# Kernel optimization log

Hardware: AMD Instinct MI355X
Metric: run time of the kernel (lower is better)

## Reference

```python
import jax, jax.numpy as jnp
import numpy as np
import math

N_HEAD = 16  # from init_kwargs

def setup_inputs() -> dict:
    key = jax.random.key(0)
    ks = jax.random.split(key, 11)
    B, T, D = 2, 2048, 1024
    s = 0.02
    return {
        "q": jax.random.normal(ks[0], (B, T, D), jnp.float32),
        "k": jax.random.normal(ks[1], (B, T, D), jnp.float32),
        "v": jax.random.normal(ks[2], (B, T, D), jnp.float32),
        "Wq": jax.random.normal(ks[3], (D, D), jnp.float32) * s,
        "bq": jax.random.normal(ks[4], (D,), jnp.float32) * s,
        "Wk": jax.random.normal(ks[5], (D, D), jnp.float32) * s,
        "bk": jax.random.normal(ks[6], (D,), jnp.float32) * s,
        "Wv": jax.random.normal(ks[7], (D, D), jnp.float32) * s,
        "bv": jax.random.normal(ks[8], (D,), jnp.float32) * s,
        "Wc": jax.random.normal(ks[9], (D, D), jnp.float32) * s,
        "bc": jax.random.normal(ks[10], (D,), jnp.float32) * s,
    }

def reference(q, k, v, Wq, bq, Wk, bk, Wv, bv, Wc, bc):
    B, T, D = q.shape
    H = N_HEAD
    nd = D // H

    def proj(x, W, b):
        # torch Linear: x @ W.T + b; then split heads -> [b, h, t, nd]
        y = x @ W.T + b
        return y.reshape(B, T, H, nd).transpose(0, 2, 1, 3)

    qh = proj(q, Wq, bq)
    kh = proj(k, Wk, bk)
    vh = proj(v, Wv, bv)

    # scores: [b, h, t_q, t_k]
    z = jnp.einsum('bhqd,bhkd->bhqk', qh, kh) / math.sqrt(nd)
    mask = jnp.tril(jnp.ones((T, T), dtype=bool))  # causal
    z = jnp.where(mask, z, -jnp.inf)
    # NOTE: original uses nn.Softmax(dim=-2) -> softmax over the QUERY axis
    attn = jax.nn.softmax(z, axis=-2)
    out = jnp.einsum('bhqk,bhkd->bhqd', attn, vh)  # [b, h, t, nd]
    out = out.transpose(0, 2, 1, 3).reshape(B, T, D)
    return out @ Wc.T + bc
```

## Files before the change

kernel.cpp:

```cpp
#include <hip/hip_runtime.h>


#define Dd 1024
#define Tt 2048
#define Bb 2
#define Hh 16
#define NDh 64
#define Mm (Bb * Tt)

using u16 = unsigned short;
using u32 = unsigned int;
typedef __attribute__((ext_vector_type(8))) short bf16x8;
typedef __attribute__((ext_vector_type(4))) float f32x4;

__device__ __forceinline__ u16 f2bf(float f) {
  return (u16)((__float_as_uint(f) + 0x8000u) >> 16);
}
__device__ __forceinline__ float fexp2(float x) {
  return __builtin_amdgcn_exp2f(x);
}
__device__ __forceinline__ void ldsdma16(const u16* g, u16* l) {
  __builtin_amdgcn_global_load_lds(
      (const __attribute__((address_space(1))) u32*)g,
      (__attribute__((address_space(3))) u32*)l, 16, 0, 0);
}
#define MFMA(a, b, c) __builtin_amdgcn_mfma_f32_16x16x32_bf16((a), (b), (c), 0, 0, 0)
__device__ __forceinline__ bf16x8 ldfrag(const u16* lds, int row, int kgrp) {
  return *(const bf16x8*)(lds + row * 64 + (((kgrp) ^ (row & 7)) * 8));
}

__global__ __launch_bounds__(256) void cvt_all(
    const float* __restrict__ w0, const float* __restrict__ w1,
    const float* __restrict__ w2, const float* __restrict__ w3,
    const float* __restrict__ q, const float* __restrict__ k,
    const float* __restrict__ v,
    u16* __restrict__ Wb, u16* __restrict__ Xb,
    float* __restrict__ outz, float* __restrict__ lsumz)
{
  const int vid = blockIdx.x * 256 + threadIdx.x;
  const float* s;
  u16* d;
  if (vid < (1 << 20)) {
    const int seg = vid >> 18, off = (vid & 0x3FFFF) * 4;
    s = (seg == 0 ? w0 : seg == 1 ? w1 : seg == 2 ? w2 : w3) + off;
    d = Wb + (size_t)seg * Dd * Dd + off;
    *(float4*)(outz + (size_t)vid * 4) = make_float4(0.f, 0.f, 0.f, 0.f);
    if (vid < Bb * Hh * Tt / 4)
      *(float4*)(lsumz + (size_t)vid * 4) = make_float4(0.f, 0.f, 0.f, 0.f);
  } else {
    const int iv = vid - (1 << 20);
    const int seg = iv >> 20, off = (iv & 0xFFFFF) * 4;
    s = (seg == 0 ? q : seg == 1 ? k : v) + off;
    d = Xb + (size_t)seg * Mm * Dd + off;
  }
  float4 f = *(const float4*)s;
  ushort4 o;
  o.x = f2bf(f.x); o.y = f2bf(f.y); o.z = f2bf(f.z); o.w = f2bf(f.w);
  *(ushort4*)d = o;
}

__device__ __forceinline__ void gemm_body(
    const u16* __restrict__ X, const u16* __restrict__ WB,
    const float* __restrict__ bias, void* Yv, float oscale,
    int omode, int kc, int knum, u16* As, u16* Bs)
{
  const int t = threadIdx.x, lane = t & 63, w = t >> 6;
  const int col = lane & 15, quad = lane >> 4;
  const int m0 = blockIdx.x * 128, n0 = blockIdx.y * 128;
  const int wm = (w >> 1) * 64, wn = (w & 1) * 64;
  const int drr = lane >> 3, dsw = ((lane & 7) ^ drr) * 8;
  const int kbeg = (Dd / knum) * kc, kend = kbeg + Dd / knum;

  f32x4 acc[4][4] = {};

  for (int k0 = kbeg; k0 < kend; k0 += 64) {
    __syncthreads();
#pragma unroll
    for (int i = 0; i < 4; i++) {
      const int rr = w * 32 + i * 8;
      ldsdma16(X + (size_t)(m0 + rr + drr) * Dd + k0 + dsw, As + rr * 64);
      ldsdma16(WB + (size_t)(n0 + rr + drr) * Dd + k0 + dsw, Bs + rr * 64);
    }
    __syncthreads();
#pragma unroll
    for (int s = 0; s < 2; s++) {
      bf16x8 a[4], b[4];
#pragma unroll
      for (int i = 0; i < 4; i++)
        a[i] = ldfrag(As, wm + i * 16 + col, s * 4 + quad);
#pragma unroll
      for (int j = 0; j < 4; j++)
        b[j] = ldfrag(Bs, wn + j * 16 + col, s * 4 + quad);
#pragma unroll
      for (int i = 0; i < 4; i++)
#pragma unroll
        for (int j = 0; j < 4; j++)
          acc[i][j] = MFMA(a[i], b[j], acc[i][j]);
    }
  }

#pragma unroll
  for (int jt = 0; jt < 4; jt++) {
    const int n = n0 + wn + jt * 16 + col;
    const float bn = (omode == 2 && kc != 0) ? 0.f : bias[n];
    if (omode == 1) {
#pragma unroll
      for (int i = 0; i < 4; i++) {
        const int mg = m0 + wm + i * 16 + quad * 4;
        const int bb = mg >> 11, tl = mg & 2047;
        ushort4 o;
        o.x = f2bf(acc[i][jt][0] + bn);
        o.y = f2bf(acc[i][jt][1] + bn);
        o.z = f2bf(acc[i][jt][2] + bn);
        o.w = f2bf(acc[i][jt][3] + bn);
        *(ushort4*)((u16*)Yv + (size_t)bb * Dd * Tt + (size_t)n * Tt + tl) = o;
      }
    } else if (omode == 0) {
      u16* Y = (u16*)Yv;
#pragma unroll
      for (int i = 0; i < 4; i++)
#pragma unroll
        for (int r = 0; r < 4; r++) {
          const int m = m0 + wm + i * 16 + quad * 4 + r;
          Y[(size_t)m * Dd + n] = f2bf((acc[i][jt][r] + bn) * oscale);
        }
    } else {
      float* Y = (float*)Yv;
#pragma unroll
      for (int i = 0; i < 4; i++)
#pragma unroll
        for (int r = 0; r < 4; r++) {
          const int m = m0 + wm + i * 16 + quad * 4 + r;
          atomicAdd(&Y[(size_t)m * Dd + n], acc[i][jt][r] + bn);
        }
    }
  }
}

__global__ __launch_bounds__(256) void proj_qkv(
    const u16* __restrict__ Xb, const u16* __restrict__ Wb,
    const float* __restrict__ bq, const float* __restrict__ bk,
    const float* __restrict__ bv,
    u16* __restrict__ Qp, u16* __restrict__ Kp, u16* __restrict__ VtG)
{
  __shared__ u16 As[128 * 64];
  __shared__ u16 Bs[128 * 64];
  const int z = blockIdx.z;
  const u16* X = Xb + (size_t)z * Mm * Dd;
  const u16* W = Wb + (size_t)z * Dd * Dd;
  const float* bias = z == 0 ? bq : z == 1 ? bk : bv;
  void* Y = z == 0 ? (void*)Qp : z == 1 ? (void*)Kp : (void*)VtG;
  const float qs = 0.125f * 1.44269504088896f;
  gemm_body(X, W, bias, Y, z == 0 ? qs : 1.0f, z == 2 ? 1 : 0, 0, 1, As, Bs);
}

__global__ __launch_bounds__(256) void gemm_final(
    const u16* __restrict__ Ctx, const u16* __restrict__ Wcb,
    const float* __restrict__ bc, float* __restrict__ out)
{
  __shared__ u16 As[128 * 64];
  __shared__ u16 Bs[128 * 64];
  gemm_body(Ctx, Wcb, bc, out, 1.0f, 2, blockIdx.z, 2, As, Bs);
}

__global__ __launch_bounds__(256) void cvt_ctx(
    const float* __restrict__ Ctx32, u16* __restrict__ Ctxb)
{
  const int vid = blockIdx.x * 256 + threadIdx.x;
  float4 f = *(const float4*)(Ctx32 + (size_t)vid * 4);
  ushort4 o;
  o.x = f2bf(f.x); o.y = f2bf(f.y); o.z = f2bf(f.z); o.w = f2bf(f.w);
  *(ushort4*)(Ctxb + (size_t)vid * 4) = o;
}

__global__ __launch_bounds__(256) void attn_stats(
    const u16* __restrict__ Qp, const u16* __restrict__ Kp,
    float* __restrict__ lsum, float* __restrict__ Ctx32z)
{
  __shared__ u16 Ks[128 * 64];
  __shared__ u16 Qs[128 * 64];
  const int t = threadIdx.x, lane = t & 63, w = t >> 6;
  const int col = lane & 15, quad = lane >> 4;
  const int bh = blockIdx.x, b = bh >> 4, h = bh & 15;
  const int j = blockIdx.y, tk0 = j * 128, c = blockIdx.z;
  const u16* Kbase = Kp + (size_t)b * Tt * Dd + h * NDh;
  const u16* Qbase = Qp + (size_t)b * Tt * Dd + h * NDh;
  const int drr = lane >> 3, dsw = ((lane & 7) ^ drr) * 8;

  {
    const size_t zid = ((size_t)(blockIdx.z * gridDim.y + blockIdx.y) * gridDim.x
                        + blockIdx.x) * 256 + t;
#pragma unroll
    for (int i = 0; i < 4; i++)
      *(float4*)(Ctx32z + (zid + (size_t)i * 262144) * 4) =
          make_float4(0.f, 0.f, 0.f, 0.f);
  }

#pragma unroll
  for (int i = 0; i < 4; i++) {
    const int rr = w * 32 + i * 8;
    ldsdma16(Kbase + (size_t)(tk0 + rr + drr) * Dd + dsw, Ks + rr * 64);
  }
  __syncthreads();
  bf16x8 ka[2][2];
#pragma unroll
  for (int s2 = 0; s2 < 2; s2++) {
    const int row = w * 32 + s2 * 16 + col;
    ka[s2][0] = ldfrag(Ks, row, quad);
    ka[s2][1] = ldfrag(Ks, row, 4 + quad);
  }

  float l[2][4] = {};

  for (int jj = j + c; jj < Tt / 128; jj += 2) {
    const bool masked = (jj == j);
    const int tq0 = jj * 128;
    __syncthreads();
#pragma unroll
    for (int i = 0; i < 4; i++) {
      const int rr = w * 32 + i * 8;
      ldsdma16(Qbase + (size_t)(tq0 + rr + drr) * Dd + dsw, Qs + rr * 64);
    }
    __syncthreads();
#pragma unroll
    for (int jt = 0; jt < 8; jt++) {
      bf16x8 qb0 = ldfrag(Qs, jt * 16 + col, quad);
      bf16x8 qb1 = ldfrag(Qs, jt * 16 + col, 4 + quad);
      const int tq = tq0 + jt * 16 + col;
#pragma unroll
      for (int s2 = 0; s2 < 2; s2++) {
        f32x4 z = {};
        z = MFMA(ka[s2][0], qb0, z);
        z = MFMA(ka[s2][1], qb1, z);
#pragma unroll
        for (int r = 0; r < 4; r++) {
          float e = fexp2(z[r]);
          if (masked) {
            const int tk = tk0 + w * 32 + s2 * 16 + quad * 4 + r;
            e = (tq >= tk) ? e : 0.f;
          }
          l[s2][r] += e;
        }
      }
    }
  }

#pragma unroll
  for (int s2 = 0; s2 < 2; s2++)
#pragma unroll
    for (int r = 0; r < 4; r++) {
      float s = l[s2][r];
#pragma unroll
      for (int m = 1; m < 16; m <<= 1) s += __shfl_xor(s, m);
      if (col == 0)
        atomicAdd(&lsum[(size_t)bh * Tt + tk0 + w * 32 + s2 * 16 + quad * 4 + r], s);
    }
}

__global__ __launch_bounds__(256) void attn_out(
    const u16* __restrict__ Qp, const u16* __restrict__ Kp,
    const u16* __restrict__ VtG, const float* __restrict__ lsum,
    float* __restrict__ Ctx32)
{
  __shared__ u16 QPs[128 * 64];
  __shared__ u16 Ks[64 * 64];
  __shared__ u16 Vts[64 * 64];
  __shared__ float srl[64];
  const int t = threadIdx.x, lane = t & 63, w = t >> 6;
  const int col = lane & 15, quad = lane >> 4;
  const int bh = blockIdx.x, b = bh >> 4, h = bh & 15;
  const int tq0 = (gridDim.y - 1 - blockIdx.y) * 128;
  const int c = blockIdx.z;
  const u16* Qbase = Qp + (size_t)b * Tt * Dd + h * NDh;
  const u16* Kbase = Kp + (size_t)b * Tt * Dd + h * NDh;
  const u16* Vbase = VtG + (size_t)b * Dd * Tt + (size_t)h * NDh * Tt;
  const int drr = lane >> 3, dsw = ((lane & 7) ^ drr) * 8;

#pragma unroll
  for (int i = 0; i < 4; i++) {
    const int rr = w * 32 + i * 8;
    ldsdma16(Qbase + (size_t)(tq0 + rr + drr) * Dd + dsw, QPs + rr * 64);
  }
  __syncthreads();
  bf16x8 qa[2][2];
#pragma unroll
  for (int s2 = 0; s2 < 2; s2++) {
    const int row = w * 32 + s2 * 16 + col;
    qa[s2][0] = ldfrag(QPs, row, quad);
    qa[s2][1] = ldfrag(QPs, row, 4 + quad);
  }

  f32x4 o[2][4] = {};

  for (int it = c; it * 64 < tq0 + 128; it += 2) {
    const int tk0 = it * 64;
    const bool masked = (tk0 >= tq0);
    __syncthreads();
#pragma unroll
    for (int i = 0; i < 2; i++) {
      const int rr = w * 16 + i * 8;
      ldsdma16(Kbase + (size_t)(tk0 + rr + drr) * Dd + dsw, Ks + rr * 64);
      ldsdma16(Vbase + (size_t)(rr + drr) * Tt + tk0 + dsw, Vts + rr * 64);
    }
    if (t < 64) srl[t] = 1.0f / lsum[(size_t)bh * Tt + tk0 + t];
    __syncthreads();
#pragma unroll
    for (int jt = 0; jt < 4; jt++) {
      bf16x8 kb0 = ldfrag(Ks, jt * 16 + col, quad);
      bf16x8 kb1 = ldfrag(Ks, jt * 16 + col, 4 + quad);
      const int tkl = jt * 16 + col;
      const float rl = srl[tkl];
#pragma unroll
      for (int s2 = 0; s2 < 2; s2++) {
        f32x4 z = {};
        z = MFMA(qa[s2][0], kb0, z);
        z = MFMA(qa[s2][1], kb1, z);
#pragma unroll
        for (int r = 0; r < 4; r++) {
          const int row = w * 32 + s2 * 16 + quad * 4 + r;
          float p = fexp2(z[r]) * rl;
          if (masked) p = (tk0 + tkl <= tq0 + row) ? p : 0.f;
          QPs[row * 64 + (((tkl >> 3) ^ (row & 7)) * 8) + (tkl & 7)] = f2bf(p);
        }
      }
    }
    bf16x8 pa[2][2];
#pragma unroll
    for (int s2 = 0; s2 < 2; s2++) {
      const int row = w * 32 + s2 * 16 + col;
      pa[s2][0] = ldfrag(QPs, row, quad);
      pa[s2][1] = ldfrag(QPs, row, 4 + quad);
    }
#pragma unroll
    for (int dn = 0; dn < 4; dn++) {
      bf16x8 vb0 = ldfrag(Vts, dn * 16 + col, quad);
      bf16x8 vb1 = ldfrag(Vts, dn * 16 + col, 4 + quad);
#pragma unroll
      for (int s2 = 0; s2 < 2; s2++) {
        o[s2][dn] = MFMA(pa[s2][0], vb0, o[s2][dn]);
        o[s2][dn] = MFMA(pa[s2][1], vb1, o[s2][dn]);
      }
    }
  }

#pragma unroll
  for (int s2 = 0; s2 < 2; s2++)
#pragma unroll
    for (int dn = 0; dn < 4; dn++)
#pragma unroll
      for (int r = 0; r < 4; r++) {
        const int tq = tq0 + w * 32 + s2 * 16 + quad * 4 + r;
        atomicAdd(&Ctx32[(size_t)(b * Tt + tq) * Dd + h * NDh + dn * 16 + col],
                  o[s2][dn][r]);
      }
}

extern "C" void kernel_launch(void* const* d_in, const int* in_sizes, int n_in,
                              void* d_out, int out_size, void* d_ws, size_t ws_size,
                              hipStream_t stream)
{
  const float* q  = (const float*)d_in[0];
  const float* k  = (const float*)d_in[1];
  const float* v  = (const float*)d_in[2];
  const float* Wq = (const float*)d_in[3];
  const float* bq = (const float*)d_in[4];
  const float* Wk = (const float*)d_in[5];
  const float* bk = (const float*)d_in[6];
  const float* Wv = (const float*)d_in[7];
  const float* bv = (const float*)d_in[8];
  const float* Wc = (const float*)d_in[9];
  const float* bc = (const float*)d_in[10];

  u16* Wb   = (u16*)d_ws;
  u16* Xb   = Wb + (size_t)4 * Dd * Dd;
  float* Ctx32 = (float*)Xb;
  u16* Qp   = Xb + (size_t)3 * Mm * Dd;
  u16* Kp   = Qp + (size_t)Mm * Dd;
  u16* VtG  = Kp + (size_t)Mm * Dd;
  u16* Ctxb = VtG + (size_t)Mm * Dd;
  float* lsum = (float*)(Ctxb + (size_t)Mm * Dd);

  cvt_all<<<16384, 256, 0, stream>>>(Wq, Wk, Wv, Wc, q, k, v, Wb, Xb,
                                     (float*)d_out, lsum);
  proj_qkv<<<dim3(Mm / 128, Dd / 128, 3), 256, 0, stream>>>(
      Xb, Wb, bq, bk, bv, Qp, Kp, VtG);
  attn_stats<<<dim3(Bb * Hh, Tt / 128, 2), 256, 0, stream>>>(Qp, Kp, lsum, Ctx32);
  attn_out<<<dim3(Bb * Hh, Tt / 128, 2), 256, 0, stream>>>(Qp, Kp, VtG, lsum, Ctx32);
  cvt_ctx<<<4096, 256, 0, stream>>>(Ctx32, Ctxb);
  gemm_final<<<dim3(Mm / 128, Dd / 128, 2), 256, 0, stream>>>(
      Ctxb, Wb + (size_t)3 * Dd * Dd, bc, (float*)d_out);
}
```

Baseline: 270.5 us.

## Fold softmax normalizer into V and replace ctx atomics with split buffers

```diff
diff --git a/kernel.cpp b/kernel.cpp
--- a/kernel.cpp
+++ b/kernel.cpp
@@ -19,6 +19,8 @@
 __device__ __forceinline__ float fexp2(float x) {
   return __builtin_amdgcn_exp2f(x);
 }
+__device__ __forceinline__ float bfl(u32 u) { return __uint_as_float(u << 16); }
+__device__ __forceinline__ float bfh(u32 u) { return __uint_as_float(u & 0xffff0000u); }
 __device__ __forceinline__ void ldsdma16(const u16* g, u16* l) {
   __builtin_amdgcn_global_load_lds(
       (const __attribute__((address_space(1))) u32*)g,
@@ -163,19 +165,45 @@
   gemm_body(Ctx, Wcb, bc, out, 1.0f, 2, blockIdx.z, 2, As, Bs);
 }
 
+__global__ __launch_bounds__(256) void vscale(
+    u16* __restrict__ Vt, const float* __restrict__ lsum)
+{
+  const size_t gid = ((size_t)blockIdx.x * 256 + threadIdx.x) * 8;
+  const int row = (int)(gid >> 11);
+  const int tt = (int)(gid & 2047);
+  const int b = row >> 10, hd = row & 1023;
+  const float* lp = lsum + (size_t)(b * Hh + (hd >> 6)) * Tt + tt;
+  uint4 v = *(const uint4*)(Vt + gid);
+  float4 l0 = *(const float4*)lp;
+  float4 l1 = *(const float4*)(lp + 4);
+  float r0 = __builtin_amdgcn_rcpf(l0.x), r1 = __builtin_amdgcn_rcpf(l0.y);
+  float r2 = __builtin_amdgcn_rcpf(l0.z), r3 = __builtin_amdgcn_rcpf(l0.w);
+  float r4 = __builtin_amdgcn_rcpf(l1.x), r5 = __builtin_amdgcn_rcpf(l1.y);
+  float r6 = __builtin_amdgcn_rcpf(l1.z), r7 = __builtin_amdgcn_rcpf(l1.w);
+  uint4 o;
+  o.x = (u32)f2bf(bfl(v.x) * r0) | ((u32)f2bf(bfh(v.x) * r1) << 16);
+  o.y = (u32)f2bf(bfl(v.y) * r2) | ((u32)f2bf(bfh(v.y) * r3) << 16);
+  o.z = (u32)f2bf(bfl(v.z) * r4) | ((u32)f2bf(bfh(v.z) * r5) << 16);
+  o.w = (u32)f2bf(bfl(v.w) * r6) | ((u32)f2bf(bfh(v.w) * r7) << 16);
+  *(uint4*)(Vt + gid) = o;
+}
+
 __global__ __launch_bounds__(256) void cvt_ctx(
-    const float* __restrict__ Ctx32, u16* __restrict__ Ctxb)
+    const float* __restrict__ Ca, const float* __restrict__ Cb,
+    u16* __restrict__ Ctxb)
 {
   const int vid = blockIdx.x * 256 + threadIdx.x;
-  float4 f = *(const float4*)(Ctx32 + (size_t)vid * 4);
+  float4 a = *(const float4*)(Ca + (size_t)vid * 4);
+  float4 b = *(const float4*)(Cb + (size_t)vid * 4);
   ushort4 o;
-  o.x = f2bf(f.x); o.y = f2bf(f.y); o.z = f2bf(f.z); o.w = f2bf(f.w);
+  o.x = f2bf(a.x + b.x); o.y = f2bf(a.y + b.y);
+  o.z = f2bf(a.z + b.z); o.w = f2bf(a.w + b.w);
   *(ushort4*)(Ctxb + (size_t)vid * 4) = o;
 }
 
 __global__ __launch_bounds__(256) void attn_stats(
     const u16* __restrict__ Qp, const u16* __restrict__ Kp,
-    float* __restrict__ lsum, float* __restrict__ Ctx32z)
+    float* __restrict__ lsum)
 {
   __shared__ u16 Ks[128 * 64];
   __shared__ u16 Qs[128 * 64];
@@ -187,15 +215,6 @@
   const u16* Qbase = Qp + (size_t)b * Tt * Dd + h * NDh;
   const int drr = lane >> 3, dsw = ((lane & 7) ^ drr) * 8;
 
-  {
-    const size_t zid = ((size_t)(blockIdx.z * gridDim.y + blockIdx.y) * gridDim.x
-                        + blockIdx.x) * 256 + t;
-#pragma unroll
-    for (int i = 0; i < 4; i++)
-      *(float4*)(Ctx32z + (zid + (size_t)i * 262144) * 4) =
-          make_float4(0.f, 0.f, 0.f, 0.f);
-  }
-
 #pragma unroll
   for (int i = 0; i < 4; i++) {
     const int rr = w * 32 + i * 8;
@@ -259,18 +278,18 @@
 
 __global__ __launch_bounds__(256) void attn_out(
     const u16* __restrict__ Qp, const u16* __restrict__ Kp,
-    const u16* __restrict__ VtG, const float* __restrict__ lsum,
-    float* __restrict__ Ctx32)
+    const u16* __restrict__ VtG,
+    float* __restrict__ Ca, float* __restrict__ Cb)
 {
   __shared__ u16 QPs[128 * 64];
   __shared__ u16 Ks[64 * 64];
   __shared__ u16 Vts[64 * 64];
-  __shared__ float srl[64];
   const int t = threadIdx.x, lane = t & 63, w = t >> 6;
   const int col = lane & 15, quad = lane >> 4;
   const int bh = blockIdx.x, b = bh >> 4, h = bh & 15;
   const int tq0 = (gridDim.y - 1 - blockIdx.y) * 128;
   const int c = blockIdx.z;
+  float* dst = c == 0 ? Ca : Cb;
   const u16* Qbase = Qp + (size_t)b * Tt * Dd + h * NDh;
   const u16* Kbase = Kp + (size_t)b * Tt * Dd + h * NDh;
   const u16* Vbase = VtG + (size_t)b * Dd * Tt + (size_t)h * NDh * Tt;
@@ -302,14 +321,12 @@
       ldsdma16(Kbase + (size_t)(tk0 + rr + drr) * Dd + dsw, Ks + rr * 64);
       ldsdma16(Vbase + (size_t)(rr + drr) * Tt + tk0 + dsw, Vts + rr * 64);
     }
-    if (t < 64) srl[t] = 1.0f / lsum[(size_t)bh * Tt + tk0 + t];
     __syncthreads();
 #pragma unroll
     for (int jt = 0; jt < 4; jt++) {
       bf16x8 kb0 = ldfrag(Ks, jt * 16 + col, quad);
       bf16x8 kb1 = ldfrag(Ks, jt * 16 + col, 4 + quad);
       const int tkl = jt * 16 + col;
-      const float rl = srl[tkl];
 #pragma unroll
       for (int s2 = 0; s2 < 2; s2++) {
         f32x4 z = {};
@@ -318,7 +335,7 @@
 #pragma unroll
         for (int r = 0; r < 4; r++) {
           const int row = w * 32 + s2 * 16 + quad * 4 + r;
-          float p = fexp2(z[r]) * rl;
+          float p = fexp2(z[r]);
           if (masked) p = (tk0 + tkl <= tq0 + row) ? p : 0.f;
           QPs[row * 64 + (((tkl >> 3) ^ (row & 7)) * 8) + (tkl & 7)] = f2bf(p);
         }
@@ -350,8 +367,7 @@
 #pragma unroll
       for (int r = 0; r < 4; r++) {
         const int tq = tq0 + w * 32 + s2 * 16 + quad * 4 + r;
-        atomicAdd(&Ctx32[(size_t)(b * Tt + tq) * Dd + h * NDh + dn * 16 + col],
-                  o[s2][dn][r]);
+        dst[(size_t)(b * Tt + tq) * Dd + h * NDh + dn * 16 + col] = o[s2][dn][r];
       }
 }
 
@@ -373,20 +389,23 @@
 
   u16* Wb   = (u16*)d_ws;
   u16* Xb   = Wb + (size_t)4 * Dd * Dd;
-  float* Ctx32 = (float*)Xb;
+  float* Ctx32a = (float*)Xb;
   u16* Qp   = Xb + (size_t)3 * Mm * Dd;
   u16* Kp   = Qp + (size_t)Mm * Dd;
   u16* VtG  = Kp + (size_t)Mm * Dd;
   u16* Ctxb = VtG + (size_t)Mm * Dd;
   float* lsum = (float*)(Ctxb + (size_t)Mm * Dd);
+  float* Ctx32b = lsum + (size_t)Bb * Hh * Tt;
 
   cvt_all<<<16384, 256, 0, stream>>>(Wq, Wk, Wv, Wc, q, k, v, Wb, Xb,
                                      (float*)d_out, lsum);
   proj_qkv<<<dim3(Mm / 128, Dd / 128, 3), 256, 0, stream>>>(
       Xb, Wb, bq, bk, bv, Qp, Kp, VtG);
-  attn_stats<<<dim3(Bb * Hh, Tt / 128, 2), 256, 0, stream>>>(Qp, Kp, lsum, Ctx32);
-  attn_out<<<dim3(Bb * Hh, Tt / 128, 2), 256, 0, stream>>>(Qp, Kp, VtG, lsum, Ctx32);
-  cvt_ctx<<<4096, 256, 0, stream>>>(Ctx32, Ctxb);
+  attn_stats<<<dim3(Bb * Hh, Tt / 128, 2), 256, 0, stream>>>(Qp, Kp, lsum);
+  vscale<<<Mm * Dd / 2048, 256, 0, stream>>>(VtG, lsum);
+  attn_out<<<dim3(Bb * Hh, Tt / 128, 2), 256, 0, stream>>>(
+      Qp, Kp, VtG, Ctx32a, Ctx32b);
+  cvt_ctx<<<4096, 256, 0, stream>>>(Ctx32a, Ctx32b, Ctxb);
   gemm_final<<<dim3(Mm / 128, Dd / 128, 2), 256, 0, stream>>>(
       Ctxb, Wb + (size_t)3 * Dd * Dd, bc, (float*)d_out);
 }
```

Measured after the change: 271.7 us. Within noise of the previous version (+0.4%).
